# Kernel optimization log

Hardware: AMD Instinct MI355X
Metric: run time of the kernel (lower is better)

The kernel has to match this reference:

```python
import jax, jax.numpy as jnp
import numpy as np

N_ATOMS = 100000
N_EDGES = 6400000

def setup_inputs() -> dict:
    key = jax.random.key(0)
    k1, k2, k3 = jax.random.split(key, 3)
    R = jax.random.normal(k1, (N_ATOMS, 3), dtype=jnp.float32)
    idx_i = jax.random.randint(k2, (N_EDGES,), 0, N_ATOMS, dtype=jnp.int64)
    idx_j = jax.random.randint(k3, (N_EDGES,), 0, N_ATOMS, dtype=jnp.int64)
    return {"R": R, "idx_i": idx_i, "idx_j": idx_j}

def reference(R, idx_i, idx_j):
    # Gather coordinates at both ends of each edge, subtract, L2 norm over xyz.
    Rij = R[idx_i] - R[idx_j]            # [E, 3]
    d_ij = jnp.sqrt(jnp.sum(Rij * Rij, axis=-1))  # [E]
    return d_ij
```

## Files before the change

kernel.cpp:

```cpp
#include <hip/hip_runtime.h>
#include <hip/hip_bf16.h>


typedef int   v4i __attribute__((ext_vector_type(4)));
typedef float v4f __attribute__((ext_vector_type(4)));

__global__ __launch_bounds__(256) void pad_R_kernel(
    const float* __restrict__ R, float* __restrict__ R4, int n_atoms)
{
    const int i = blockIdx.x * blockDim.x + threadIdx.x;
    if (i < n_atoms) {
        const float x = R[3 * i + 0];
        const float y = R[3 * i + 1];
        const float z = R[3 * i + 2];
        v4f v = {x, y, z, 0.0f};
        *(v4f*)(R4 + 4 * (size_t)i) = v;
    }
}

__device__ __forceinline__ v4f gather_sc0(const float* base, int idx)
{
    v4f r;
    const int voff = idx << 4;
    asm volatile("global_load_dwordx4 %0, %1, %2 sc0"
                 : "=v"(r)
                 : "v"(voff), "s"(base)
                 : "memory");
    return r;
}

__device__ __forceinline__ float dist3(v4f a, v4f b)
{
    const v4f d = a - b;
    return sqrtf(d.x * d.x + d.y * d.y + d.z * d.z);
}

__global__ __launch_bounds__(256) void pairwise_dist_kernel(
    const float* __restrict__ R4,
    const int* __restrict__ idx_i,
    const int* __restrict__ idx_j,
    float* __restrict__ out,
    int n_oct)
{
    const int t = blockIdx.x * blockDim.x + threadIdx.x;
    if (t >= n_oct) return;

    const v4i a0 = ((const v4i*)idx_i)[2 * t + 0];
    const v4i a1 = ((const v4i*)idx_i)[2 * t + 1];
    const v4i b0 = ((const v4i*)idx_j)[2 * t + 0];
    const v4i b1 = ((const v4i*)idx_j)[2 * t + 1];

    v4f pa0 = gather_sc0(R4, a0.x), pb0 = gather_sc0(R4, b0.x);
    v4f pa1 = gather_sc0(R4, a0.y), pb1 = gather_sc0(R4, b0.y);
    v4f pa2 = gather_sc0(R4, a0.z), pb2 = gather_sc0(R4, b0.z);
    v4f pa3 = gather_sc0(R4, a0.w), pb3 = gather_sc0(R4, b0.w);
    v4f pa4 = gather_sc0(R4, a1.x), pb4 = gather_sc0(R4, b1.x);
    v4f pa5 = gather_sc0(R4, a1.y), pb5 = gather_sc0(R4, b1.y);
    v4f pa6 = gather_sc0(R4, a1.z), pb6 = gather_sc0(R4, b1.z);
    v4f pa7 = gather_sc0(R4, a1.w), pb7 = gather_sc0(R4, b1.w);

    asm volatile("s_waitcnt vmcnt(0)"
                 : "+v"(pa0), "+v"(pb0), "+v"(pa1), "+v"(pb1),
                   "+v"(pa2), "+v"(pb2), "+v"(pa3), "+v"(pb3),
                   "+v"(pa4), "+v"(pb4), "+v"(pa5), "+v"(pb5),
                   "+v"(pa6), "+v"(pb6), "+v"(pa7), "+v"(pb7)
                 :
                 : "memory");

    v4f o0, o1;
    o0.x = dist3(pa0, pb0);
    o0.y = dist3(pa1, pb1);
    o0.z = dist3(pa2, pb2);
    o0.w = dist3(pa3, pb3);
    o1.x = dist3(pa4, pb4);
    o1.y = dist3(pa5, pb5);
    o1.z = dist3(pa6, pb6);
    o1.w = dist3(pa7, pb7);

    ((v4f*)out)[2 * t + 0] = o0;
    ((v4f*)out)[2 * t + 1] = o1;
}

__global__ __launch_bounds__(64) void pairwise_dist_tail_kernel(
    const float* __restrict__ R4,
    const int* __restrict__ idx_i,
    const int* __restrict__ idx_j,
    float* __restrict__ out,
    int start, int n_edges)
{
    const int e = start + blockIdx.x * blockDim.x + threadIdx.x;
    if (e < n_edges) {
        const v4f pa = *(const v4f*)(R4 + 4 * (size_t)idx_i[e]);
        const v4f pb = *(const v4f*)(R4 + 4 * (size_t)idx_j[e]);
        out[e] = dist3(pa, pb);
    }
}

extern "C" void kernel_launch(void* const* d_in, const int* in_sizes, int n_in,
                              void* d_out, int out_size, void* d_ws, size_t ws_size,
                              hipStream_t stream)
{
    const float* R     = (const float*)d_in[0];
    const int*   idx_i = (const int*)d_in[1];
    const int*   idx_j = (const int*)d_in[2];
    float*       out   = (float*)d_out;

    const int n_atoms = in_sizes[0] / 3;
    const int n_edges = in_sizes[1];
    float*    R4      = (float*)d_ws;

    {
        const int block = 256;
        const int grid  = (n_atoms + block - 1) / block;
        pad_R_kernel<<<grid, block, 0, stream>>>(R, R4, n_atoms);
    }

    const int n_oct = n_edges >> 3;
    {
        const int block = 256;
        const int grid  = (n_oct + block - 1) / block;
        pairwise_dist_kernel<<<grid, block, 0, stream>>>(R4, idx_i, idx_j, out, n_oct);
    }

    const int tail_start = n_oct << 3;
    if (tail_start < n_edges) {
        const int tail = n_edges - tail_start;
        pairwise_dist_tail_kernel<<<(tail + 63) / 64, 64, 0, stream>>>(
            R4, idx_i, idx_j, out, tail_start, n_edges);
    }
}
```

Before: 145.1 us.

## Route half of coordinate gathers through direct global-to-LDS loads

Half of the random coordinate gathers (the idx_j side) now use global_load_lds to write straight into per-wave shared memory, while the idx_i side still loads into registers. The index and output accesses are also remapped so each block handles 2048 edges with coalesced strided vec4 loads. The aim is to lower VGPR pressure and spread the gather traffic across two load paths to get more memory parallelism. In exchange it adds 32KB of LDS per block, which can limit occupancy, plus extra LDS reads.

```diff
diff --git a/kernel.cpp b/kernel.cpp
--- a/kernel.cpp
+++ b/kernel.cpp
@@ -29,6 +29,14 @@
     return r;
 }
 
+__device__ __forceinline__ void gather_to_lds(const float* gaddr, float* lbase)
+{
+    __builtin_amdgcn_global_load_lds(
+        (const __attribute__((address_space(1))) void*)gaddr,
+        (__attribute__((address_space(3))) void*)lbase,
+        16, 0, 0);
+}
+
 __device__ __forceinline__ float dist3(v4f a, v4f b)
 {
     const v4f d = a - b;
@@ -39,33 +47,50 @@
     const float* __restrict__ R4,
     const int* __restrict__ idx_i,
     const int* __restrict__ idx_j,
-    float* __restrict__ out,
-    int n_oct)
+    float* __restrict__ out)
 {
-    const int t = blockIdx.x * blockDim.x + threadIdx.x;
-    if (t >= n_oct) return;
+    __shared__ float lds[4 * 8 * 256];
+    const int tid  = threadIdx.x;
+    const int lane = tid & 63;
+    const int wave = tid >> 6;
+    float* wbase = &lds[wave * 8 * 256];
 
-    const v4i a0 = ((const v4i*)idx_i)[2 * t + 0];
-    const v4i a1 = ((const v4i*)idx_i)[2 * t + 1];
-    const v4i b0 = ((const v4i*)idx_j)[2 * t + 0];
-    const v4i b1 = ((const v4i*)idx_j)[2 * t + 1];
+    const int q0 = blockIdx.x * 512 + tid;
+    const int q1 = q0 + 256;
 
-    v4f pa0 = gather_sc0(R4, a0.x), pb0 = gather_sc0(R4, b0.x);
-    v4f pa1 = gather_sc0(R4, a0.y), pb1 = gather_sc0(R4, b0.y);
-    v4f pa2 = gather_sc0(R4, a0.z), pb2 = gather_sc0(R4, b0.z);
-    v4f pa3 = gather_sc0(R4, a0.w), pb3 = gather_sc0(R4, b0.w);
-    v4f pa4 = gather_sc0(R4, a1.x), pb4 = gather_sc0(R4, b1.x);
-    v4f pa5 = gather_sc0(R4, a1.y), pb5 = gather_sc0(R4, b1.y);
-    v4f pa6 = gather_sc0(R4, a1.z), pb6 = gather_sc0(R4, b1.z);
-    v4f pa7 = gather_sc0(R4, a1.w), pb7 = gather_sc0(R4, b1.w);
+    const v4i a0 = ((const v4i*)idx_i)[q0];
+    const v4i a1 = ((const v4i*)idx_i)[q1];
+    const v4i b0 = ((const v4i*)idx_j)[q0];
+    const v4i b1 = ((const v4i*)idx_j)[q1];
 
-    asm volatile("s_waitcnt vmcnt(0)"
-                 : "+v"(pa0), "+v"(pb0), "+v"(pa1), "+v"(pb1),
-                   "+v"(pa2), "+v"(pb2), "+v"(pa3), "+v"(pb3),
-                   "+v"(pa4), "+v"(pb4), "+v"(pa5), "+v"(pb5),
-                   "+v"(pa6), "+v"(pb6), "+v"(pa7), "+v"(pb7)
-                 :
-                 : "memory");
+    gather_to_lds(R4 + 4 * (size_t)b0.x, wbase + 0 * 256);
+    gather_to_lds(R4 + 4 * (size_t)b0.y, wbase + 1 * 256);
+    gather_to_lds(R4 + 4 * (size_t)b0.z, wbase + 2 * 256);
+    gather_to_lds(R4 + 4 * (size_t)b0.w, wbase + 3 * 256);
+    gather_to_lds(R4 + 4 * (size_t)b1.x, wbase + 4 * 256);
+    gather_to_lds(R4 + 4 * (size_t)b1.y, wbase + 5 * 256);
+    gather_to_lds(R4 + 4 * (size_t)b1.z, wbase + 6 * 256);
+    gather_to_lds(R4 + 4 * (size_t)b1.w, wbase + 7 * 256);
+
+    v4f pa0 = gather_sc0(R4, a0.x);
+    v4f pa1 = gather_sc0(R4, a0.y);
+    v4f pa2 = gather_sc0(R4, a0.z);
+    v4f pa3 = gather_sc0(R4, a0.w);
+    v4f pa4 = gather_sc0(R4, a1.x);
+    v4f pa5 = gather_sc0(R4, a1.y);
+    v4f pa6 = gather_sc0(R4, a1.z);
+    v4f pa7 = gather_sc0(R4, a1.w);
+
+    asm volatile("s_waitcnt vmcnt(0)" ::: "memory");
+
+    const v4f pb0 = *(const v4f*)(wbase + 0 * 256 + lane * 4);
+    const v4f pb1 = *(const v4f*)(wbase + 1 * 256 + lane * 4);
+    const v4f pb2 = *(const v4f*)(wbase + 2 * 256 + lane * 4);
+    const v4f pb3 = *(const v4f*)(wbase + 3 * 256 + lane * 4);
+    const v4f pb4 = *(const v4f*)(wbase + 4 * 256 + lane * 4);
+    const v4f pb5 = *(const v4f*)(wbase + 5 * 256 + lane * 4);
+    const v4f pb6 = *(const v4f*)(wbase + 6 * 256 + lane * 4);
+    const v4f pb7 = *(const v4f*)(wbase + 7 * 256 + lane * 4);
 
     v4f o0, o1;
     o0.x = dist3(pa0, pb0);
@@ -77,8 +102,8 @@
     o1.z = dist3(pa6, pb6);
     o1.w = dist3(pa7, pb7);
 
-    ((v4f*)out)[2 * t + 0] = o0;
-    ((v4f*)out)[2 * t + 1] = o1;
+    ((v4f*)out)[q0] = o0;
+    ((v4f*)out)[q1] = o1;
 }
 
 __global__ __launch_bounds__(64) void pairwise_dist_tail_kernel(
@@ -115,17 +140,16 @@
         pad_R_kernel<<<grid, block, 0, stream>>>(R, R4, n_atoms);
     }
 
-    const int n_oct = n_edges >> 3;
-    {
-        const int block = 256;
-        const int grid  = (n_oct + block - 1) / block;
-        pairwise_dist_kernel<<<grid, block, 0, stream>>>(R4, idx_i, idx_j, out, n_oct);
+    const int n_full_blocks = n_edges / 2048;
+    if (n_full_blocks > 0) {
+        pairwise_dist_kernel<<<n_full_blocks, 256, 0, stream>>>(
+            R4, idx_i, idx_j, out);
     }
 
-    const int tail_start = n_oct << 3;
-    if (tail_start < n_edges) {
-        const int tail = n_edges - tail_start;
+    const int done = n_full_blocks * 2048;
+    if (done < n_edges) {
+        const int tail = n_edges - done;
         pairwise_dist_tail_kernel<<<(tail + 63) / 64, 64, 0, stream>>>(
-            R4, idx_i, idx_j, out, tail_start, n_edges);
+            R4, idx_i, idx_j, out, done, n_edges);
     }
 }
```

Result: no change. 145.6 us (+0.4%).
